# Kernel tuning notes

Hardware: AMD Instinct MI355X
Metric: run time of the kernel (lower is better)

## Reference

```python
import jax, jax.numpy as jnp
import numpy as np
from jax import lax

B, N, C, H = 16, 577, 1024, 16
D = C // H          # head_dim = 64
M = 24              # spatial side, M*M = N-1
CH = C // 4         # conv bottleneck channels = 256
EPS = 1e-5


def _ln(x, g, b):
    mu = jnp.mean(x, axis=-1, keepdims=True)
    var = jnp.mean((x - mu) ** 2, axis=-1, keepdims=True)
    return (x - mu) * lax.rsqrt(var + EPS) * g + b


def setup_inputs() -> dict:
    key = jax.random.key(0)
    ks = jax.random.split(key, 8)
    s = 0.02
    return {
        "x": jax.random.normal(ks[0], (B, N, C), jnp.float32),
        "ln1_g": jnp.ones((C,), jnp.float32),
        "ln1_b": jnp.zeros((C,), jnp.float32),
        "in_w": jax.random.normal(ks[1], (3 * C, C), jnp.float32) * s,
        "in_b": jnp.zeros((3 * C,), jnp.float32),
        "out_w": jax.random.normal(ks[2], (C, C), jnp.float32) * s,
        "out_b": jnp.zeros((C,), jnp.float32),
        "ln2_g": jnp.ones((C,), jnp.float32),
        "ln2_b": jnp.zeros((C,), jnp.float32),
        "conv1_w": jax.random.normal(ks[3], (CH, C, 3, 3), jnp.float32) * s,
        "conv1_b": jnp.zeros((CH,), jnp.float32),
        "conv2_w": jax.random.normal(ks[4], (C, CH, 3, 3), jnp.float32) * s,
        "conv2_b": jnp.zeros((C,), jnp.float32),
    }


def reference(x, ln1_g, ln1_b, in_w, in_b, out_w, out_b, ln2_g, ln2_b,
              conv1_w, conv1_b, conv2_w, conv2_b):
    residual = x
    h = _ln(x, ln1_g, ln1_b)
    # qkv projection: (B,N,3C) -> (3,B,H,N,D)
    qkv = (h @ in_w.T + in_b).reshape(B, N, 3, H, D).transpose(2, 0, 3, 1, 4)
    q, k, v = qkv[0], qkv[1], qkv[2]
    scale = D ** (-0.5)
    scores = jnp.einsum("bhnd,bhmd->bhnm", q, k) * scale   # (B,H,N,N)
    attn = jax.nn.softmax(scores, axis=-1)
    o = jnp.einsum("bhnm,bhmd->bhnd", attn, v)
    o = o.transpose(0, 2, 1, 3).reshape(B, N, C)
    o = o @ out_w.T + out_b
    x = o + residual                                       # first residual

    y = _ln(x, ln2_g, ln2_b)
    f = y[:, :-1, :].reshape(B, M, M, C).transpose(0, 3, 1, 2)   # NCHW
    c = y[:, -1:, :]                                             # class token
    f = lax.conv_general_dilated(f, conv1_w, (1, 1), "SAME",
                                 dimension_numbers=("NCHW", "OIHW", "NCHW"))
    f = jax.nn.gelu(f + conv1_b[None, :, None, None])
    f = lax.conv_general_dilated(f, conv2_w, (1, 1), "SAME",
                                 dimension_numbers=("NCHW", "OIHW", "NCHW"))
    f = f + conv2_b[None, :, None, None]
    f = f.transpose(0, 2, 3, 1).reshape(B, N - 1, C)
    y = jnp.concatenate((f, c), axis=1)
    return x + y
```

## Files before the change

### kernel.cpp

```cpp
#include <hip/hip_runtime.h>

typedef unsigned short u16;
typedef unsigned int u32;
typedef __bf16 bf16x8 __attribute__((ext_vector_type(8)));
typedef float f32x4 __attribute__((ext_vector_type(4)));

#define DEVI __device__ __forceinline__

#define BB 16
#define NN 577
#define CC 1024
#define HH 16
#define DD 64
#define BN 9232
#define PIX 576
#define WW 24
#define CHN 256
#define VROW 584
#define PSZ (9216 * 256)

DEVI u16 f2b(float f) {
  u32 u = __builtin_bit_cast(u32, f);
  u32 r = 0x7FFFu + ((u >> 16) & 1u);
  return (u16)((u + r) >> 16);
}

DEVI float b2f(u16 h) { return __builtin_bit_cast(float, (u32)h << 16); }

DEVI bf16x8 ldfrag(const u16* p) {
  uint4 u = *(const uint4*)p;
  return __builtin_bit_cast(bf16x8, u);
}

DEVI f32x4 mfma16(bf16x8 a, bf16x8 b, f32x4 c) {
  return __builtin_amdgcn_mfma_f32_16x16x32_bf16(a, b, c, 0, 0, 0);
}

DEVI void gld_lds16(const u16* g, u16* l) {
  __builtin_amdgcn_global_load_lds((const __attribute__((address_space(1))) void*)g,
                                   (__attribute__((address_space(3))) void*)l, 16, 0, 0);
}

DEVI float gelu_tanh(float v) {
  const float x3 = v * v * v;
  const float t = __expf(1.5957691216057308f * (v + 0.044715f * x3));
  const float th = (t - 1.f) / (t + 1.f);
  return 0.5f * v * (1.f + th);
}

__global__ __launch_bounds__(256) void prep_kernel(
    const float* __restrict__ in_w, const float* __restrict__ out_w,
    const float* __restrict__ c1w, const float* __restrict__ c2w,
    u16* __restrict__ wqkv, u16* __restrict__ wout,
    u16* __restrict__ w1t, u16* __restrict__ w2t, u16* __restrict__ zpad) {
  const int i0 = blockIdx.x * 256 + threadIdx.x;
  const int stride = gridDim.x * 256;
  for (int i = i0; i < 3072 * 1024; i += stride) wqkv[i] = f2b(in_w[i]);
  for (int i = i0; i < 1024 * 1024; i += stride) wout[i] = f2b(out_w[i]);
  for (int i = i0; i < 256 * 9216; i += stride) {
    int oc = i / 9216, rem = i - oc * 9216, tap = rem >> 10, c = rem & 1023;
    w1t[i] = f2b(c1w[(size_t)oc * 9216 + c * 9 + tap]);
  }
  for (int i = i0; i < 1024 * 2304; i += stride) {
    int oc = i / 2304, rem = i - oc * 2304, tap = rem >> 8, c = rem & 255;
    w2t[i] = f2b(c2w[(size_t)oc * 2304 + c * 9 + tap]);
  }
  if (i0 < 128) zpad[i0] = 0;
}

template <int MODE>
__global__ __launch_bounds__(256) void ln_kernel(
    const float* __restrict__ xf, const u16* __restrict__ xh,
    const float* __restrict__ gam, const float* __restrict__ bet,
    u16* __restrict__ yout, float* __restrict__ oextra) {
  __shared__ float sh[8];
  const int row = blockIdx.x;
  const int tid = threadIdx.x;
  float4 v;
  if constexpr (MODE == 0) {
    v = ((const float4*)(xf + (size_t)row * CC))[tid];
  } else {
    ushort4 uv = ((const ushort4*)(xh + (size_t)row * CC))[tid];
    v = make_float4(b2f(uv.x), b2f(uv.y), b2f(uv.z), b2f(uv.w));
  }
  float s = v.x + v.y + v.z + v.w;
  float qq = v.x * v.x + v.y * v.y + v.z * v.z + v.w * v.w;
#pragma unroll
  for (int off = 32; off > 0; off >>= 1) {
    s += __shfl_down(s, off);
    qq += __shfl_down(qq, off);
  }
  if ((tid & 63) == 0) { sh[tid >> 6] = s; sh[4 + (tid >> 6)] = qq; }
  __syncthreads();
  s = sh[0] + sh[1] + sh[2] + sh[3];
  qq = sh[4] + sh[5] + sh[6] + sh[7];
  const float mu = s * (1.f / 1024.f);
  const float rstd = rsqrtf(qq * (1.f / 1024.f) - mu * mu + 1e-5f);
  const float4 g4 = ((const float4*)gam)[tid];
  const float4 b4 = ((const float4*)bet)[tid];
  const float o0 = (v.x - mu) * rstd * g4.x + b4.x;
  const float o1 = (v.y - mu) * rstd * g4.y + b4.y;
  const float o2 = (v.z - mu) * rstd * g4.z + b4.z;
  const float o3 = (v.w - mu) * rstd * g4.w + b4.w;
  ushort4 st = make_ushort4(f2b(o0), f2b(o1), f2b(o2), f2b(o3));
  *(ushort4*)(yout + (size_t)row * CC + tid * 4) = st;
  if constexpr (MODE == 1) {
    if (row % NN == NN - 1) {
      float4 ov = make_float4(v.x + o0, v.y + o1, v.z + o2, v.w + o3);
      ((float4*)(oextra + (size_t)row * CC))[tid] = ov;
    }
  }
}

struct GArgs {
  const u16* A; const u16* Bm; const float* bias; const float* res; const u16* resH;
  float* outF; u16* outH; u16* outQ; u16* outK; u16* outV; const u16* zpad;
  int M, K;
};

__global__ __launch_bounds__(512, 1) void qkv_kernel(GArgs ag) {
  __shared__ u16 SH[65536];
  const int tid = threadIdx.x;
  const int w = tid >> 6, l = tid & 63;
  const int wm = w >> 2, wn = w & 3;
  const int lr = l & 15, lg = l >> 4;
  const int orig = blockIdx.x;
  const int xcd = orig & 7;
  const int wg = (xcd < 4 ? xcd * 56 : 224 + (xcd - 4) * 55) + (orig >> 3);
  const int nt = wg / 37, mt = wg - nt * 37;
  const int m0 = mt * 256, n0 = nt * 256;

  const int srow = tid >> 3;
  const int schk = tid & 7;

  auto stageA = [&](int buf, int kt, int j) {
    const int row = j * 64 + srow;
    const int ch = schk ^ (row & 7);
    int m = m0 + row;
    m = m < ag.M ? m : ag.M - 1;
    gld_lds16(ag.A + (size_t)m * 1024 + kt * 64 + ch * 8,
              &SH[buf * 16384 + (j * 64 + w * 8) * 64]);
  };
  auto stageB = [&](int buf, int kt, int j) {
    const int row = j * 64 + srow;
    const int ch = schk ^ (row & 7);
    gld_lds16(ag.Bm + (size_t)(n0 + row) * 1024 + kt * 64 + ch * 8,
              &SH[32768 + buf * 16384 + (j * 64 + w * 8) * 64]);
  };

  f32x4 acc[8][4] = {};

#pragma unroll
  for (int j = 0; j < 4; ++j) { stageA(0, 0, j); stageB(0, 0, j); }

  for (int kt = 0; kt < 16; ++kt) {
    asm volatile("s_waitcnt vmcnt(0)" ::: "memory");
    __builtin_amdgcn_s_barrier();
    const int bf = kt & 1, nb = bf ^ 1;
    const u16* AB = &SH[bf * 16384];
    const u16* BBm = &SH[32768 + bf * 16384];
    bf16x8 bfr[4];
#pragma unroll
    for (int ph = 0; ph < 4; ++ph) {
      const int mg = (ph & 1) << 2;
      const int kh = ph >> 1;
      bf16x8 af[4];
#pragma unroll
      for (int i = 0; i < 4; ++i) {
        const int ra = wm * 128 + (mg + i) * 16 + lr;
        af[i] = ldfrag(&AB[ra * 64 + (((kh << 2) + lg) ^ (ra & 7)) * 8]);
      }
      if ((ph & 1) == 0) {
#pragma unroll
        for (int i = 0; i < 4; ++i) {
          const int rb = wn * 64 + i * 16 + lr;
          bfr[i] = ldfrag(&BBm[rb * 64 + (((kh << 2) + lg) ^ (rb & 7)) * 8]);
        }
      }
      if (kt + 1 < 16) {
        stageA(nb, kt + 1, ph);
        stageB(nb, kt + 1, ph);
      }
      __builtin_amdgcn_s_barrier();
      asm volatile("s_waitcnt lgkmcnt(0)" ::: "memory");
      __builtin_amdgcn_s_setprio(1);
#pragma unroll
      for (int mi = 0; mi < 4; ++mi)
#pragma unroll
        for (int ni = 0; ni < 4; ++ni)
          acc[mg + mi][ni] = mfma16(af[mi], bfr[ni], acc[mg + mi][ni]);
      __builtin_amdgcn_s_setprio(0);
      __builtin_amdgcn_s_barrier();
    }
  }

  if (n0 >= 2048) {
    __syncthreads();
    const int hh = (n0 + wn * 64 - 2048) >> 6;
    u16* scr = SH + w * 5120;
#pragma unroll
    for (int qh = 0; qh < 2; ++qh) {
      if (qh) { asm volatile("s_waitcnt lgkmcnt(0)" ::: "memory"); }
      const int G0 = m0 + wm * 128 + qh * 64;
      const int b0q = G0 / NN;
      const bool ok = (G0 + 63 < ag.M) && (b0q == (G0 + 63) / NN);
      if (ok) {
#pragma unroll
        for (int mi = 0; mi < 4; ++mi) {
#pragma unroll
          for (int ni = 0; ni < 4; ++ni) {
            const f32x4 a4 = acc[qh * 4 + mi][ni];
            const float bv = ag.bias[n0 + wn * 64 + ni * 16 + lr];
            ushort4 st;
            st.x = f2b(a4[0] + bv);
            st.y = f2b(a4[1] + bv);
            st.z = f2b(a4[2] + bv);
            st.w = f2b(a4[3] + bv);
            *(ushort4*)(scr + (ni * 16 + lr) * 80 + mi * 16 + lg * 4) = st;
          }
        }
        asm volatile("s_waitcnt lgkmcnt(0)" ::: "memory");
        const int nb2 = G0 - b0q * NN;
        u16* vb = ag.outV + (size_t)((b0q * 16 + hh) * 64) * VROW;
#pragma unroll
        for (int pass = 0; pass < 8; ++pass) {
          const int d_ = pass * 8 + (l >> 3);
          const int nn = (l & 7) * 8;
          uint4 vv = *(const uint4*)(scr + d_ * 80 + nn);
          u16* dst = vb + (size_t)d_ * VROW + nb2 + nn;
          if (!(nb2 & 1)) {
            ((u32*)dst)[0] = vv.x; ((u32*)dst)[1] = vv.y;
            ((u32*)dst)[2] = vv.z; ((u32*)dst)[3] = vv.w;
          } else {
            u16 tmp[8];
            *(uint4*)tmp = vv;
#pragma unroll
            for (int j = 0; j < 8; ++j) dst[j] = tmp[j];
          }
        }
      } else {
#pragma unroll
        for (int mi = 0; mi < 4; ++mi) {
#pragma unroll
          for (int r = 0; r < 4; ++r) {
            const int row = G0 + mi * 16 + lg * 4 + r;
            if (row >= ag.M) continue;
            const int b = row / NN, n = row - b * NN;
#pragma unroll
            for (int ni = 0; ni < 4; ++ni) {
              const int col = n0 + wn * 64 + ni * 16 + lr;
              const int d = col & 63;
              const float v = acc[qh * 4 + mi][ni][r] + ag.bias[col];
              ag.outV[((size_t)((b * 16 + hh) * 64 + d)) * VROW + n] = f2b(v);
            }
          }
        }
      }
    }
    return;
  }
  const bool isQ = n0 < 1024;
#pragma unroll
  for (int mi = 0; mi < 8; ++mi) {
#pragma unroll
    for (int r = 0; r < 4; ++r) {
      const int row = m0 + wm * 128 + mi * 16 + (lg << 2) + r;
      if (row >= ag.M) continue;
      const int b = row / NN, n = row - b * NN;
#pragma unroll
      for (int ni = 0; ni < 4; ++ni) {
        const int col = n0 + wn * 64 + ni * 16 + lr;
        const int hd = col & 1023, h = hd >> 6, d = hd & 63;
        const float v = acc[mi][ni][r] + ag.bias[col];
        if (isQ)
          ag.outQ[((size_t)(b * 16 + h) * NN + n) * DD + d] = f2b(v * 0.18033688011112042f);
        else
          ag.outK[((size_t)(b * 16 + h) * NN + n) * DD + d] = f2b(v);
      }
    }
  }
}

template <int MODE>
__global__ __launch_bounds__(256) void gemm_kernel(GArgs ag) {
  __shared__ u16 SH[24576];
  const int tid = threadIdx.x;
  const int w = tid >> 6, l = tid & 63;
  const int wr = w >> 1, wc = w & 1;
  const int lr = l & 15, lg = l >> 4;
  const int bid = blockIdx.x;
  int mt, nt, tapz = 0;
  if constexpr (MODE == 1 || MODE == 3) {
    nt = bid & 7; mt = bid >> 3;
  } else {
    const int g = (bid & 7) * 162 + (bid >> 3);
    tapz = g / 144;
    const int rem = g - tapz * 144;
    nt = rem / 72; mt = rem - nt * 72;
  }
  const int m0 = mt * 128, n0 = nt * 128;
  const int rA = w * 16 + (l >> 2);
  const int cbs = ((l & 3) ^ ((l >> 3) & 3)) * 8;

  auto stage = [&](int buf, int kt) {
    const int k0 = kt * 32;
    u16* Ald = SH + buf * 4096;
    u16* Bld = SH + 12288 + buf * 4096;
#pragma unroll
    for (int c = 0; c < 2; ++c) {
      const int r = c * 64 + rA;
      const u16* asrc;
      if constexpr (MODE == 1) {
        int m = m0 + r;
        m = m < ag.M ? m : ag.M - 1;
        asrc = ag.A + (size_t)m * ag.K + (k0 + cbs);
      } else {
        const int m = m0 + r;
        const int b = m / PIX, p = m - b * PIX;
        const int py = p / WW, px = p - py * WW;
        constexpr int CKc = (MODE == 3) ? 256 : 1024;
        const int tap = (MODE == 4) ? tapz : (k0 / CKc);
        const int c0 = (MODE == 4) ? k0 : (k0 - tap * CKc);
        const int py2 = py + (tap / 3) - 1, px2 = px + (tap % 3) - 1;
        if ((u32)py2 < (u32)WW && (u32)px2 < (u32)WW) {
          if constexpr (MODE == 4)
            asrc = ag.A + ((size_t)(b * NN + py2 * WW + px2) * CC + c0 + cbs);
          else
            asrc = ag.A + ((size_t)(b * PIX + py2 * WW + px2) * CHN + c0 + cbs);
        } else {
          asrc = ag.zpad + cbs;
        }
      }
      gld_lds16(asrc, &Ald[c * 2048 + w * 512]);
      const u16* bsrc;
      if constexpr (MODE == 4)
        bsrc = ag.Bm + (size_t)(n0 + r) * 9216 + (tapz * 1024 + k0 + cbs);
      else
        bsrc = ag.Bm + (size_t)(n0 + r) * ag.K + (k0 + cbs);
      gld_lds16(bsrc, &Bld[c * 2048 + w * 512]);
    }
  };

  f32x4 acc[4][4] = {};
  const int KL = (MODE == 4) ? 1024 : ag.K;
  const int nst = KL >> 5;

  stage(0, 0);
  stage(1, 1);

  const int swz = (lr >> 1) & 3;
  int b0 = 0, b1 = 1, b2 = 2;
  for (int kt = 0; kt < nst; ++kt) {
    if (kt + 1 < nst) { asm volatile("s_waitcnt vmcnt(4)" ::: "memory"); }
    else              { asm volatile("s_waitcnt vmcnt(0)" ::: "memory"); }
    __builtin_amdgcn_s_barrier();
    if (kt + 2 < nst) stage(b2, kt + 2);
    bf16x8 af[4], bfr[4];
#pragma unroll
    for (int i = 0; i < 4; ++i)
      af[i] = ldfrag(&SH[b0 * 4096 + (wr * 64 + i * 16 + lr) * 32 + ((lg ^ swz) * 8)]);
#pragma unroll
    for (int i = 0; i < 4; ++i)
      bfr[i] = ldfrag(&SH[12288 + b0 * 4096 + (wc * 64 + i * 16 + lr) * 32 + ((lg ^ swz) * 8)]);
    __builtin_amdgcn_s_setprio(1);
#pragma unroll
    for (int mi = 0; mi < 4; ++mi)
#pragma unroll
      for (int ni = 0; ni < 4; ++ni) acc[mi][ni] = mfma16(af[mi], bfr[ni], acc[mi][ni]);
    __builtin_amdgcn_s_setprio(0);
    const int tmp = b0; b0 = b1; b1 = b2; b2 = tmp;
  }

#pragma unroll
  for (int mi = 0; mi < 4; ++mi) {
#pragma unroll
    for (int r = 0; r < 4; ++r) {
      const int row = m0 + wr * 64 + mi * 16 + lg * 4 + r;
      if (row >= ag.M) continue;
#pragma unroll
      for (int ni = 0; ni < 4; ++ni) {
        const int col = n0 + wc * 64 + ni * 16 + lr;
        if constexpr (MODE == 4) {
          u16* pb = (tapz < 5) ? ag.outH : ag.outQ;
          const int tl = (tapz < 5) ? tapz : tapz - 5;
          pb[(size_t)tl * PSZ + (size_t)row * CHN + col] = f2b(acc[mi][ni][r]);
        } else if constexpr (MODE == 1) {
          const size_t idx = (size_t)row * CC + col;
          ag.outH[idx] = f2b(acc[mi][ni][r] + ag.bias[col] + ag.res[idx]);
        } else {
          const int b = row / PIX, p = row - b * PIX;
          const size_t idx = (size_t)(b * NN + p) * CC + col;
          ag.outF[idx] = acc[mi][ni][r] + ag.bias[col] + b2f(ag.resH[idx]);
        }
      }
    }
  }
}

__global__ __launch_bounds__(256) void gelu_reduce_kernel(
    const u16* __restrict__ pA, const u16* __restrict__ pB,
    const float* __restrict__ bias, u16* __restrict__ f1) {
  const size_t i4 = ((size_t)blockIdx.x * 256 + threadIdx.x) * 4;
  const int col = (int)(i4 & 255);
  float s0 = 0.f, s1 = 0.f, s2 = 0.f, s3 = 0.f;
#pragma unroll
  for (int t = 0; t < 5; ++t) {
    ushort4 u = *(const ushort4*)(pA + (size_t)t * PSZ + i4);
    s0 += b2f(u.x); s1 += b2f(u.y); s2 += b2f(u.z); s3 += b2f(u.w);
  }
#pragma unroll
  for (int t = 0; t < 4; ++t) {
    ushort4 u = *(const ushort4*)(pB + (size_t)t * PSZ + i4);
    s0 += b2f(u.x); s1 += b2f(u.y); s2 += b2f(u.z); s3 += b2f(u.w);
  }
  const float4 b4 = *(const float4*)(bias + col);
  ushort4 st = make_ushort4(f2b(gelu_tanh(s0 + b4.x)), f2b(gelu_tanh(s1 + b4.y)),
                            f2b(gelu_tanh(s2 + b4.z)), f2b(gelu_tanh(s3 + b4.w)));
  *(ushort4*)(f1 + i4) = st;
}

__global__ __launch_bounds__(512) void attn_kernel(
    const u16* __restrict__ q, const u16* __restrict__ k,
    const u16* __restrict__ vt, u16* __restrict__ o) {
  __shared__ u16 SH2[24576];
  const int tid = threadIdx.x;
  const int w = tid >> 6, l = tid & 63;
  const int lr = l & 15, lg = l >> 4;
  const int lg4 = lg * 4;
  const int bid = blockIdx.x;
  const int xcd = bid & 7, gg = bid >> 3;
  const int bh = (gg / 5) * 8 + xcd;
  const int qt = gg % 5;
  const int b = bh >> 4, h = bh & 15;

  const u16* qp = q + (size_t)bh * NN * DD;
  const u16* kp = k + (size_t)bh * NN * DD;
  const u16* vp = vt + (size_t)bh * DD * VROW;

  const int qrow = qt * 128 + w * 16 + lr;
  const int qrc = qrow < NN ? qrow : NN - 1;
  const bf16x8 qf0 = ldfrag(qp + (size_t)qrc * DD + lg * 8);
  const bf16x8 qf1 = ldfrag(qp + (size_t)qrc * DD + 32 + lg * 8);

  const int srow = l >> 3;
  const int schk = (l & 7) ^ (srow & 7);
  auto stage = [&](int buf, int kt) {
    const int kb = kt * 64;
    gld_lds16(kp + (size_t)(kb + w * 8 + srow) * DD + schk * 8,
              &SH2[buf * 4096 + w * 512]);
    gld_lds16(vp + (size_t)(w * 8 + srow) * VROW + kb + schk * 8,
              &SH2[8192 + buf * 4096 + w * 512]);
  };

  f32x4 oa[4] = {};
  float mrow = -1e30f;
  float lsum = 0.f;
  u16* pw = &SH2[16384 + w * 1024];
  const int x7 = lr & 7;
  const int x3 = lr & 3;

  stage(0, 0);
  stage(1, 1);

  for (int kt = 0; kt < 10; ++kt) {
    if (kt <= 7) { asm volatile("s_waitcnt vmcnt(2)" ::: "memory"); }
    else         { asm volatile("s_waitcnt vmcnt(0)" ::: "memory"); }
    __builtin_amdgcn_s_barrier();
    const u16* KB = &SH2[(kt & 1) * 4096];
    const u16* VB = &SH2[8192 + (kt & 1) * 4096];
    const int kb = kt * 64;

    f32x4 s[4] = {};
#pragma unroll
    for (int g = 0; g < 4; ++g) {
      const int row = g * 16 + lr;
      const bf16x8 a0 = ldfrag(&KB[row * 64 + ((lg ^ x7) * 8)]);
      const bf16x8 a1 = ldfrag(&KB[row * 64 + (((4 + lg) ^ x7) * 8)]);
      s[g] = mfma16(a0, qf0, s[g]);
      s[g] = mfma16(a1, qf1, s[g]);
    }
    float t[16];
    const bool last = (kt == 9);
#pragma unroll
    for (int g = 0; g < 4; ++g)
#pragma unroll
      for (int r = 0; r < 4; ++r) {
        const int key = kb + g * 16 + lg4 + r;
        t[g * 4 + r] = (!last || key < NN) ? s[g][r] : -3e38f;
      }
    float pmax = t[0];
#pragma unroll
    for (int i = 1; i < 16; ++i) pmax = fmaxf(pmax, t[i]);
    pmax = fmaxf(pmax, __shfl_xor(pmax, 16));
    pmax = fmaxf(pmax, __shfl_xor(pmax, 32));
    if (!__all(pmax <= mrow + 8.f)) {
      const float mn = fmaxf(mrow, pmax);
      const float corr = exp2f(mrow - mn);
      mrow = mn;
      lsum *= corr;
      float bc[4];
#pragma unroll
      for (int r = 0; r < 4; ++r) bc[r] = __shfl(corr, (l & 48) | (lg4 + r));
#pragma unroll
      for (int g = 0; g < 4; ++g)
#pragma unroll
        for (int r = 0; r < 4; ++r) oa[g][r] *= bc[r];
    }
    float ps[16];
    float rsum = 0.f;
#pragma unroll
    for (int i = 0; i < 16; ++i) { ps[i] = exp2f(t[i] - mrow); rsum += ps[i]; }
    rsum += __shfl_xor(rsum, 16);
    rsum += __shfl_xor(rsum, 32);
    lsum += rsum;
#pragma unroll
    for (int g = 0; g < 4; ++g) {
      u32 w0, w1;
      asm("v_cvt_pk_bf16_f32 %0, %1, %2" : "=v"(w0) : "v"(ps[g * 4 + 0]), "v"(ps[g * 4 + 1]));
      asm("v_cvt_pk_bf16_f32 %0, %1, %2" : "=v"(w1) : "v"(ps[g * 4 + 2]), "v"(ps[g * 4 + 3]));
      const int lc = (g & 1) * 2 + (lg >> 1);
      const int off = (g >> 1) * 512 + lr * 32 + ((lc ^ x3) * 8) + (lg & 1) * 4;
      *(uint2*)(&pw[off]) = make_uint2(w0, w1);
    }
    asm volatile("s_waitcnt lgkmcnt(0)" ::: "memory");
    const bf16x8 paf = ldfrag(&pw[lr * 32 + ((lg ^ x3) * 8)]);
    const bf16x8 pbf = ldfrag(&pw[512 + lr * 32 + ((lg ^ x3) * 8)]);
#pragma unroll
    for (int dg = 0; dg < 4; ++dg) {
      const int row = dg * 16 + lr;
      const bf16x8 v0 = ldfrag(&VB[row * 64 + ((lg ^ x7) * 8)]);
      const bf16x8 v1 = ldfrag(&VB[row * 64 + (((4 + lg) ^ x7) * 8)]);
      oa[dg] = mfma16(paf, v0, oa[dg]);
      oa[dg] = mfma16(pbf, v1, oa[dg]);
    }
    asm volatile("s_waitcnt lgkmcnt(0)" ::: "memory");
    __builtin_amdgcn_s_barrier();
    if (kt + 2 <= 9) stage(kt & 1, kt + 2);
  }

  const int nq = qt * 128 + w * 16 + lg4;
  float linv[4];
#pragma unroll
  for (int r = 0; r < 4; ++r) linv[r] = __shfl(lsum, (l & 48) | (lg4 + r));
#pragma unroll
  for (int r = 0; r < 4; ++r) {
    const int n = nq + r;
    if (n >= NN) continue;
    const float inv = 1.0f / linv[r];
#pragma unroll
    for (int g = 0; g < 4; ++g)
      o[(size_t)(b * NN + n) * CC + h * DD + g * 16 + lr] = f2b(oa[g][r] * inv);
  }
}

extern "C" void kernel_launch(void* const* d_in, const int* in_sizes, int n_in,
                              void* d_out, int out_size, void* d_ws, size_t ws_size,
                              hipStream_t stream) {
  const float* x     = (const float*)d_in[0];
  const float* ln1_g = (const float*)d_in[1];
  const float* ln1_b = (const float*)d_in[2];
  const float* in_w  = (const float*)d_in[3];
  const float* in_b  = (const float*)d_in[4];
  const float* out_w = (const float*)d_in[5];
  const float* out_b = (const float*)d_in[6];
  const float* ln2_g = (const float*)d_in[7];
  const float* ln2_b = (const float*)d_in[8];
  const float* c1w   = (const float*)d_in[9];
  const float* c1b   = (const float*)d_in[10];
  const float* c2w   = (const float*)d_in[11];
  const float* c2b   = (const float*)d_in[12];
  float* out = (float*)d_out;

  char* ws = (char*)d_ws;
  size_t off = 0;
  auto alloc = [&](size_t bytes) {
    void* p = ws + off;
    off += (bytes + 255) & ~(size_t)255;
    return p;
  };
  u16* hb   = (u16*)alloc((size_t)BN * CC * 2);
  u16* wqkv = (u16*)alloc((size_t)3072 * 1024 * 2);
  u16* wout = (u16*)alloc((size_t)1024 * 1024 * 2);
  u16* w1t  = (u16*)alloc((size_t)256 * 9216 * 2);
  u16* w2t  = (u16*)alloc((size_t)1024 * 2304 * 2);
  u16* qb   = (u16*)alloc((size_t)256 * NN * DD * 2);
  u16* kb   = (u16*)alloc((size_t)256 * NN * DD * 2);
  u16* vtb  = (u16*)alloc((size_t)256 * DD * VROW * 2 + 16384);
  u16* x2h  = (u16*)alloc((size_t)BN * CC * 2);
  u16* zpad = (u16*)alloc(256);
  u16* ob = hb;
  u16* yb = qb;
  u16* f1 = kb;
  u16* pA = hb;
  u16* pB = vtb;

  prep_kernel<<<1024, 256, 0, stream>>>(in_w, out_w, c1w, c2w, wqkv, wout, w1t, w2t, zpad);
  ln_kernel<0><<<BN, 256, 0, stream>>>(x, nullptr, ln1_g, ln1_b, hb, nullptr);
  {
    GArgs a{hb, wqkv, in_b, nullptr, nullptr, nullptr, nullptr, qb, kb, vtb, zpad, BN, CC};
    qkv_kernel<<<444, 512, 0, stream>>>(a);
  }
  attn_kernel<<<1280, 512, 0, stream>>>(qb, kb, vtb, ob);
  {
    GArgs a{ob, wout, out_b, x, nullptr, nullptr, x2h, nullptr, nullptr, nullptr, zpad, BN, CC};
    gemm_kernel<1><<<584, 256, 0, stream>>>(a);
  }
  ln_kernel<1><<<BN, 256, 0, stream>>>(nullptr, x2h, ln2_g, ln2_b, yb, out);
  {
    GArgs a{yb, w1t, c1b, nullptr, nullptr, nullptr, pA, pB, nullptr, nullptr, zpad, 9216, 9216};
    gemm_kernel<4><<<1296, 256, 0, stream>>>(a);
  }
  gelu_reduce_kernel<<<2304, 256, 0, stream>>>(pA, pB, c1b, f1);
  {
    GArgs a{f1, w2t, c2b, nullptr, x2h, out, nullptr, nullptr, nullptr, nullptr, zpad, 9216, 2304};
    gemm_kernel<3><<<576, 256, 0, stream>>>(a);
  }
}
```

Measured before the change: 380.2 us.

## Move conv GEMMs to the 256x256 tile kernel with split-K and a combine pass

Generalizes the 512-thread 256x256-tile QKV GEMM into a templated kernel and runs both convolutions through it. Conv1 keeps its per-tap split (9 partials). Conv2 is split into two K pieces (5 and 4 taps) written as bf16 partials, then summed with bias and residual by a new combine kernel. The larger tiles aim to raise data reuse and MFMA efficiency over the 128x128 kernel. In exchange, conv2 now writes and rereads extra partial buffers, and rounding those partials to bf16 costs some precision.

```diff
diff --git a/kernel.cpp b/kernel.cpp
--- a/kernel.cpp
+++ b/kernel.cpp
@@ -118,7 +118,8 @@
   int M, K;
 };
 
-__global__ __launch_bounds__(512, 1) void qkv_kernel(GArgs ag) {
+template <int MODE>
+__global__ __launch_bounds__(512, 1) void gemm8_kernel(GArgs ag) {
   __shared__ u16 SH[65536];
   const int tid = threadIdx.x;
   const int w = tid >> 6, l = tid & 63;
@@ -126,26 +127,65 @@
   const int lr = l & 15, lg = l >> 4;
   const int orig = blockIdx.x;
   const int xcd = orig & 7;
-  const int wg = (xcd < 4 ? xcd * 56 : 224 + (xcd - 4) * 55) + (orig >> 3);
-  const int nt = wg / 37, mt = wg - nt * 37;
-  const int m0 = mt * 256, n0 = nt * 256;
+  int mt, nt = 0, tapz = 0, piece = 0, NST;
+  if constexpr (MODE == 0) {
+    const int wg = (xcd < 4 ? xcd * 56 : 224 + (xcd - 4) * 55) + (orig >> 3);
+    nt = wg / 37; mt = wg - nt * 37;
+    NST = 16;
+  } else if constexpr (MODE == 2) {
+    const int wg = (xcd < 4 ? xcd * 41 : 164 + (xcd - 4) * 40) + (orig >> 3);
+    tapz = wg / 36; mt = wg - tapz * 36;
+    NST = 16;
+  } else {
+    const int wg = xcd * 36 + (orig >> 3);
+    piece = wg / 144;
+    const int rem = wg - piece * 144;
+    mt = rem >> 2; nt = rem & 3;
+    NST = piece ? 16 : 20;
+  }
+  const int m0 = mt * 256, n0 = nt * ((MODE == 2) ? 0 : 256);
 
   const int srow = tid >> 3;
   const int schk = tid & 7;
 
+  auto aSrc = [&](int row, int kt) -> const u16* {
+    const int ch = schk ^ (row & 7);
+    if constexpr (MODE == 0) {
+      int m = m0 + row;
+      m = m < ag.M ? m : ag.M - 1;
+      return ag.A + (size_t)m * 1024 + kt * 64 + ch * 8;
+    } else {
+      const int m = m0 + row;
+      const int b = m / PIX, p = m - b * PIX;
+      const int py = p / WW, px = p - py * WW;
+      int tap, c0;
+      if constexpr (MODE == 2) { tap = tapz; c0 = kt * 64; }
+      else { tap = (piece ? 5 : 0) + (kt >> 2); c0 = (kt & 3) * 64; }
+      const int py2 = py + (tap / 3) - 1, px2 = px + (tap % 3) - 1;
+      if ((u32)py2 < (u32)WW && (u32)px2 < (u32)WW) {
+        if constexpr (MODE == 2)
+          return ag.A + ((size_t)(b * NN + py2 * WW + px2) * CC + c0 + ch * 8);
+        else
+          return ag.A + ((size_t)(b * PIX + py2 * WW + px2) * CHN + c0 + ch * 8);
+      }
+      return ag.zpad + ch * 8;
+    }
+  };
+  auto bSrc = [&](int row, int kt) -> const u16* {
+    const int ch = schk ^ (row & 7);
+    if constexpr (MODE == 0)
+      return ag.Bm + (size_t)(n0 + row) * 1024 + kt * 64 + ch * 8;
+    else if constexpr (MODE == 2)
+      return ag.Bm + (size_t)row * 9216 + tapz * 1024 + kt * 64 + ch * 8;
+    else
+      return ag.Bm + (size_t)(n0 + row) * 2304 + (piece ? 1280 : 0) + kt * 64 + ch * 8;
+  };
+
   auto stageA = [&](int buf, int kt, int j) {
-    const int row = j * 64 + srow;
-    const int ch = schk ^ (row & 7);
-    int m = m0 + row;
-    m = m < ag.M ? m : ag.M - 1;
-    gld_lds16(ag.A + (size_t)m * 1024 + kt * 64 + ch * 8,
-              &SH[buf * 16384 + (j * 64 + w * 8) * 64]);
+    gld_lds16(aSrc(j * 64 + srow, kt), &SH[buf * 16384 + (j * 64 + w * 8) * 64]);
   };
   auto stageB = [&](int buf, int kt, int j) {
-    const int row = j * 64 + srow;
-    const int ch = schk ^ (row & 7);
-    gld_lds16(ag.Bm + (size_t)(n0 + row) * 1024 + kt * 64 + ch * 8,
-              &SH[32768 + buf * 16384 + (j * 64 + w * 8) * 64]);
+    gld_lds16(bSrc(j * 64 + srow, kt), &SH[32768 + buf * 16384 + (j * 64 + w * 8) * 64]);
   };
 
   f32x4 acc[8][4] = {};
@@ -153,7 +193,7 @@
 #pragma unroll
   for (int j = 0; j < 4; ++j) { stageA(0, 0, j); stageB(0, 0, j); }
 
-  for (int kt = 0; kt < 16; ++kt) {
+  for (int kt = 0; kt < NST; ++kt) {
     asm volatile("s_waitcnt vmcnt(0)" ::: "memory");
     __builtin_amdgcn_s_barrier();
     const int bf = kt & 1, nb = bf ^ 1;
@@ -177,7 +217,7 @@
           bfr[i] = ldfrag(&BBm[rb * 64 + (((kh << 2) + lg) ^ (rb & 7)) * 8]);
         }
       }
-      if (kt + 1 < 16) {
+      if (kt + 1 < NST) {
         stageA(nb, kt + 1, ph);
         stageB(nb, kt + 1, ph);
       }
@@ -194,88 +234,121 @@
     }
   }
 
-  if (n0 >= 2048) {
-    __syncthreads();
-    const int hh = (n0 + wn * 64 - 2048) >> 6;
-    u16* scr = SH + w * 5120;
-#pragma unroll
-    for (int qh = 0; qh < 2; ++qh) {
-      if (qh) { asm volatile("s_waitcnt lgkmcnt(0)" ::: "memory"); }
-      const int G0 = m0 + wm * 128 + qh * 64;
-      const int b0q = G0 / NN;
-      const bool ok = (G0 + 63 < ag.M) && (b0q == (G0 + 63) / NN);
-      if (ok) {
-#pragma unroll
-        for (int mi = 0; mi < 4; ++mi) {
-#pragma unroll
-          for (int ni = 0; ni < 4; ++ni) {
-            const f32x4 a4 = acc[qh * 4 + mi][ni];
-            const float bv = ag.bias[n0 + wn * 64 + ni * 16 + lr];
-            ushort4 st;
-            st.x = f2b(a4[0] + bv);
-            st.y = f2b(a4[1] + bv);
-            st.z = f2b(a4[2] + bv);
-            st.w = f2b(a4[3] + bv);
-            *(ushort4*)(scr + (ni * 16 + lr) * 80 + mi * 16 + lg * 4) = st;
+  if constexpr (MODE == 2) {
+    const int tl = (tapz < 5) ? tapz : tapz - 5;
+    u16* pb = (tapz < 5) ? ag.outH : ag.outQ;
+#pragma unroll
+    for (int mi = 0; mi < 8; ++mi) {
+#pragma unroll
+      for (int r = 0; r < 4; ++r) {
+        const int row = m0 + wm * 128 + mi * 16 + (lg << 2) + r;
+#pragma unroll
+        for (int ni = 0; ni < 4; ++ni) {
+          const int col = wn * 64 + ni * 16 + lr;
+          pb[(size_t)tl * PSZ + (size_t)row * CHN + col] = f2b(acc[mi][ni][r]);
+        }
+      }
+    }
+    return;
+  } else if constexpr (MODE == 3) {
+    u16* pb = piece ? ag.outQ : ag.outH;
+#pragma unroll
+    for (int mi = 0; mi < 8; ++mi) {
+#pragma unroll
+      for (int r = 0; r < 4; ++r) {
+        const int row = m0 + wm * 128 + mi * 16 + (lg << 2) + r;
+#pragma unroll
+        for (int ni = 0; ni < 4; ++ni) {
+          const int col = n0 + wn * 64 + ni * 16 + lr;
+          pb[(size_t)row * CC + col] = f2b(acc[mi][ni][r]);
+        }
+      }
+    }
+    return;
+  } else {
+    if (n0 >= 2048) {
+      __syncthreads();
+      const int hh = (n0 + wn * 64 - 2048) >> 6;
+      u16* scr = SH + w * 5120;
+#pragma unroll
+      for (int qh = 0; qh < 2; ++qh) {
+        if (qh) { asm volatile("s_waitcnt lgkmcnt(0)" ::: "memory"); }
+        const int G0 = m0 + wm * 128 + qh * 64;
+        const int b0q = G0 / NN;
+        const bool ok = (G0 + 63 < ag.M) && (b0q == (G0 + 63) / NN);
+        if (ok) {
+#pragma unroll
+          for (int mi = 0; mi < 4; ++mi) {
+#pragma unroll
+            for (int ni = 0; ni < 4; ++ni) {
+              const f32x4 a4 = acc[qh * 4 + mi][ni];
+              const float bv = ag.bias[n0 + wn * 64 + ni * 16 + lr];
+              ushort4 st;
+              st.x = f2b(a4[0] + bv);
+              st.y = f2b(a4[1] + bv);
+              st.z = f2b(a4[2] + bv);
+              st.w = f2b(a4[3] + bv);
+              *(ushort4*)(scr + (ni * 16 + lr) * 80 + mi * 16 + lg * 4) = st;
+            }
           }
-        }
-        asm volatile("s_waitcnt lgkmcnt(0)" ::: "memory");
-        const int nb2 = G0 - b0q * NN;
-        u16* vb = ag.outV + (size_t)((b0q * 16 + hh) * 64) * VROW;
-#pragma unroll
-        for (int pass = 0; pass < 8; ++pass) {
-          const int d_ = pass * 8 + (l >> 3);
-          const int nn = (l & 7) * 8;
-          uint4 vv = *(const uint4*)(scr + d_ * 80 + nn);
-          u16* dst = vb + (size_t)d_ * VROW + nb2 + nn;
-          if (!(nb2 & 1)) {
-            ((u32*)dst)[0] = vv.x; ((u32*)dst)[1] = vv.y;
-            ((u32*)dst)[2] = vv.z; ((u32*)dst)[3] = vv.w;
-          } else {
-            u16 tmp[8];
-            *(uint4*)tmp = vv;
-#pragma unroll
-            for (int j = 0; j < 8; ++j) dst[j] = tmp[j];
+          asm volatile("s_waitcnt lgkmcnt(0)" ::: "memory");
+          const int nb2 = G0 - b0q * NN;
+          u16* vb = ag.outV + (size_t)((b0q * 16 + hh) * 64) * VROW;
+#pragma unroll
+          for (int pass = 0; pass < 8; ++pass) {
+            const int d_ = pass * 8 + (l >> 3);
+            const int nn = (l & 7) * 8;
+            uint4 vv = *(const uint4*)(scr + d_ * 80 + nn);
+            u16* dst = vb + (size_t)d_ * VROW + nb2 + nn;
+            if (!(nb2 & 1)) {
+              ((u32*)dst)[0] = vv.x; ((u32*)dst)[1] = vv.y;
+              ((u32*)dst)[2] = vv.z; ((u32*)dst)[3] = vv.w;
+            } else {
+              u16 tmp[8];
+              *(uint4*)tmp = vv;
+#pragma unroll
+              for (int j = 0; j < 8; ++j) dst[j] = tmp[j];
+            }
           }
-        }
-      } else {
-#pragma unroll
-        for (int mi = 0; mi < 4; ++mi) {
-#pragma unroll
-          for (int r = 0; r < 4; ++r) {
-            const int row = G0 + mi * 16 + lg * 4 + r;
-            if (row >= ag.M) continue;
-            const int b = row / NN, n = row - b * NN;
-#pragma unroll
-            for (int ni = 0; ni < 4; ++ni) {
-              const int col = n0 + wn * 64 + ni * 16 + lr;
-              const int d = col & 63;
-              const float v = acc[qh * 4 + mi][ni][r] + ag.bias[col];
-              ag.outV[((size_t)((b * 16 + hh) * 64 + d)) * VROW + n] = f2b(v);
+        } else {
+#pragma unroll
+          for (int mi = 0; mi < 4; ++mi) {
+#pragma unroll
+            for (int r = 0; r < 4; ++r) {
+              const int row = G0 + mi * 16 + lg * 4 + r;
+              if (row >= ag.M) continue;
+              const int b = row / NN, n = row - b * NN;
+#pragma unroll
+              for (int ni = 0; ni < 4; ++ni) {
+                const int col = n0 + wn * 64 + ni * 16 + lr;
+                const int d = col & 63;
+                const float v = acc[qh * 4 + mi][ni][r] + ag.bias[col];
+                ag.outV[((size_t)((b * 16 + hh) * 64 + d)) * VROW + n] = f2b(v);
+              }
             }
           }
         }
       }
-    }
-    return;
-  }
-  const bool isQ = n0 < 1024;
-#pragma unroll
-  for (int mi = 0; mi < 8; ++mi) {
-#pragma unroll
-    for (int r = 0; r < 4; ++r) {
-      const int row = m0 + wm * 128 + mi * 16 + (lg << 2) + r;
-      if (row >= ag.M) continue;
-      const int b = row / NN, n = row - b * NN;
-#pragma unroll
-      for (int ni = 0; ni < 4; ++ni) {
-        const int col = n0 + wn * 64 + ni * 16 + lr;
-        const int hd = col & 1023, h = hd >> 6, d = hd & 63;
-        const float v = acc[mi][ni][r] + ag.bias[col];
-        if (isQ)
-          ag.outQ[((size_t)(b * 16 + h) * NN + n) * DD + d] = f2b(v * 0.18033688011112042f);
-        else
-          ag.outK[((size_t)(b * 16 + h) * NN + n) * DD + d] = f2b(v);
+      return;
+    }
+    const bool isQ = n0 < 1024;
+#pragma unroll
+    for (int mi = 0; mi < 8; ++mi) {
+#pragma unroll
+      for (int r = 0; r < 4; ++r) {
+        const int row = m0 + wm * 128 + mi * 16 + (lg << 2) + r;
+        if (row >= ag.M) continue;
+        const int b = row / NN, n = row - b * NN;
+#pragma unroll
+        for (int ni = 0; ni < 4; ++ni) {
+          const int col = n0 + wn * 64 + ni * 16 + lr;
+          const int hd = col & 1023, h = hd >> 6, d = hd & 63;
+          const float v = acc[mi][ni][r] + ag.bias[col];
+          if (isQ)
+            ag.outQ[((size_t)(b * 16 + h) * NN + n) * DD + d] = f2b(v * 0.18033688011112042f);
+          else
+            ag.outK[((size_t)(b * 16 + h) * NN + n) * DD + d] = f2b(v);
+        }
       }
     }
   }
@@ -289,15 +362,7 @@
   const int wr = w >> 1, wc = w & 1;
   const int lr = l & 15, lg = l >> 4;
   const int bid = blockIdx.x;
-  int mt, nt, tapz = 0;
-  if constexpr (MODE == 1 || MODE == 3) {
-    nt = bid & 7; mt = bid >> 3;
-  } else {
-    const int g = (bid & 7) * 162 + (bid >> 3);
-    tapz = g / 144;
-    const int rem = g - tapz * 144;
-    nt = rem / 72; mt = rem - nt * 72;
-  }
+  const int nt = bid & 7, mt = bid >> 3;
   const int m0 = mt * 128, n0 = nt * 128;
   const int rA = w * 16 + (l >> 2);
   const int cbs = ((l & 3) ^ ((l >> 3) & 3)) * 8;
@@ -309,41 +374,15 @@
 #pragma unroll
     for (int c = 0; c < 2; ++c) {
       const int r = c * 64 + rA;
-      const u16* asrc;
-      if constexpr (MODE == 1) {
-        int m = m0 + r;
-        m = m < ag.M ? m : ag.M - 1;
-        asrc = ag.A + (size_t)m * ag.K + (k0 + cbs);
-      } else {
-        const int m = m0 + r;
-        const int b = m / PIX, p = m - b * PIX;
-        const int py = p / WW, px = p - py * WW;
-        constexpr int CKc = (MODE == 3) ? 256 : 1024;
-        const int tap = (MODE == 4) ? tapz : (k0 / CKc);
-        const int c0 = (MODE == 4) ? k0 : (k0 - tap * CKc);
-        const int py2 = py + (tap / 3) - 1, px2 = px + (tap % 3) - 1;
-        if ((u32)py2 < (u32)WW && (u32)px2 < (u32)WW) {
-          if constexpr (MODE == 4)
-            asrc = ag.A + ((size_t)(b * NN + py2 * WW + px2) * CC + c0 + cbs);
-          else
-            asrc = ag.A + ((size_t)(b * PIX + py2 * WW + px2) * CHN + c0 + cbs);
-        } else {
-          asrc = ag.zpad + cbs;
-        }
-      }
-      gld_lds16(asrc, &Ald[c * 2048 + w * 512]);
-      const u16* bsrc;
-      if constexpr (MODE == 4)
-        bsrc = ag.Bm + (size_t)(n0 + r) * 9216 + (tapz * 1024 + k0 + cbs);
-      else
-        bsrc = ag.Bm + (size_t)(n0 + r) * ag.K + (k0 + cbs);
-      gld_lds16(bsrc, &Bld[c * 2048 + w * 512]);
+      int m = m0 + r;
+      m = m < ag.M ? m : ag.M - 1;
+      gld_lds16(ag.A + (size_t)m * ag.K + (k0 + cbs), &Ald[c * 2048 + w * 512]);
+      gld_lds16(ag.Bm + (size_t)(n0 + r) * ag.K + (k0 + cbs), &Bld[c * 2048 + w * 512]);
     }
   };
 
   f32x4 acc[4][4] = {};
-  const int KL = (MODE == 4) ? 1024 : ag.K;
-  const int nst = KL >> 5;
+  const int nst = ag.K >> 5;
 
   stage(0, 0);
   stage(1, 1);
@@ -380,18 +419,8 @@
 #pragma unroll
       for (int ni = 0; ni < 4; ++ni) {
         const int col = n0 + wc * 64 + ni * 16 + lr;
-        if constexpr (MODE == 4) {
-          u16* pb = (tapz < 5) ? ag.outH : ag.outQ;
-          const int tl = (tapz < 5) ? tapz : tapz - 5;
-          pb[(size_t)tl * PSZ + (size_t)row * CHN + col] = f2b(acc[mi][ni][r]);
-        } else if constexpr (MODE == 1) {
-          const size_t idx = (size_t)row * CC + col;
-          ag.outH[idx] = f2b(acc[mi][ni][r] + ag.bias[col] + ag.res[idx]);
-        } else {
-          const int b = row / PIX, p = row - b * PIX;
-          const size_t idx = (size_t)(b * NN + p) * CC + col;
-          ag.outF[idx] = acc[mi][ni][r] + ag.bias[col] + b2f(ag.resH[idx]);
-        }
+        const size_t idx = (size_t)row * CC + col;
+        ag.outH[idx] = f2b(acc[mi][ni][r] + ag.bias[col] + ag.res[idx]);
       }
     }
   }
@@ -417,6 +446,27 @@
   ushort4 st = make_ushort4(f2b(gelu_tanh(s0 + b4.x)), f2b(gelu_tanh(s1 + b4.y)),
                             f2b(gelu_tanh(s2 + b4.z)), f2b(gelu_tanh(s3 + b4.w)));
   *(ushort4*)(f1 + i4) = st;
+}
+
+__global__ __launch_bounds__(256) void conv2_combine_kernel(
+    const u16* __restrict__ p0, const u16* __restrict__ p1,
+    const float* __restrict__ bias, const u16* __restrict__ x2h,
+    float* __restrict__ out) {
+  const size_t i4 = ((size_t)blockIdx.x * 256 + threadIdx.x) * 4;
+  const int col = (int)(i4 & 1023);
+  const int row = (int)(i4 >> 10);
+  const int b = row / PIX, p = row - b * PIX;
+  const ushort4 a = *(const ushort4*)(p0 + i4);
+  const ushort4 c = *(const ushort4*)(p1 + i4);
+  const size_t oidx = ((size_t)(b * NN + p) << 10) + col;
+  const ushort4 xh = *(const ushort4*)(x2h + oidx);
+  const float4 bv = *(const float4*)(bias + col);
+  float4 o;
+  o.x = b2f(a.x) + b2f(c.x) + bv.x + b2f(xh.x);
+  o.y = b2f(a.y) + b2f(c.y) + bv.y + b2f(xh.y);
+  o.z = b2f(a.z) + b2f(c.z) + bv.z + b2f(xh.z);
+  o.w = b2f(a.w) + b2f(c.w) + bv.w + b2f(xh.w);
+  *(float4*)(out + oidx) = o;
 }
 
 __global__ __launch_bounds__(512) void attn_kernel(
@@ -598,7 +648,7 @@
   ln_kernel<0><<<BN, 256, 0, stream>>>(x, nullptr, ln1_g, ln1_b, hb, nullptr);
   {
     GArgs a{hb, wqkv, in_b, nullptr, nullptr, nullptr, nullptr, qb, kb, vtb, zpad, BN, CC};
-    qkv_kernel<<<444, 512, 0, stream>>>(a);
+    gemm8_kernel<0><<<444, 512, 0, stream>>>(a);
   }
   attn_kernel<<<1280, 512, 0, stream>>>(qb, kb, vtb, ob);
   {
@@ -608,11 +658,12 @@
   ln_kernel<1><<<BN, 256, 0, stream>>>(nullptr, x2h, ln2_g, ln2_b, yb, out);
   {
     GArgs a{yb, w1t, c1b, nullptr, nullptr, nullptr, pA, pB, nullptr, nullptr, zpad, 9216, 9216};
-    gemm_kernel<4><<<1296, 256, 0, stream>>>(a);
+    gemm8_kernel<2><<<324, 512, 0, stream>>>(a);
   }
   gelu_reduce_kernel<<<2304, 256, 0, stream>>>(pA, pB, c1b, f1);
   {
-    GArgs a{f1, w2t, c2b, nullptr, x2h, out, nullptr, nullptr, nullptr, nullptr, zpad, 9216, 2304};
-    gemm_kernel<3><<<576, 256, 0, stream>>>(a);
-  }
-}
+    GArgs a{f1, w2t, c2b, nullptr, nullptr, nullptr, hb, vtb, nullptr, nullptr, zpad, 9216, 2304};
+    gemm8_kernel<3><<<288, 512, 0, stream>>>(a);
+  }
+  conv2_combine_kernel<<<9216, 256, 0, stream>>>(hb, vtb, c2b, x2h, out);
+}
```

New measurement: 382.2 us. No clear change (+0.5%).
